# Optimization experiments

Measured on AMD Instinct MI355X. Metric: run time of the kernel, lower is better.

## Reference

```python
import jax, jax.numpy as jnp
import numpy as np
import math

NH, NKV, HD = 8, 1, 128
SOFTCAP = 30.0
ROPE_BASE = 500000.0


def _rope_tables(T, hd, base):
    half = hd // 2
    inv_freq = 1.0 / (base ** (np.arange(half, dtype=np.float32) / half))
    t = np.arange(T, dtype=np.float32)
    ang = np.outer(t, inv_freq)  # [T, half]
    return jnp.asarray(np.cos(ang)), jnp.asarray(np.sin(ang))


def apply_rope(x, cos, sin):
    # x: [B, T, H, hd]; cos/sin: [T, hd//2]
    half = x.shape[-1] // 2
    x1, x2 = x[..., :half], x[..., half:]
    T = x.shape[1]
    c = cos[:T][None, :, None, :]
    s = sin[:T][None, :, None, :]
    return jnp.concatenate([x1 * c - x2 * s, x1 * s + x2 * c], axis=-1)


def setup_inputs() -> dict:
    key = jax.random.key(0)
    ks = jax.random.split(key, 5)
    B, T, D = 4, 2048, 1024
    KD = NKV * HD
    x = jax.random.normal(ks[0], (B, T, D), dtype=jnp.float32)
    Wq = jax.random.normal(ks[1], (D, D), dtype=jnp.float32) * (D ** -0.5)
    Wk = jax.random.normal(ks[2], (KD, D), dtype=jnp.float32) * (D ** -0.5)
    Wv = jax.random.normal(ks[3], (KD, D), dtype=jnp.float32) * (D ** -0.5)
    Wo = jax.random.normal(ks[4], (D, D), dtype=jnp.float32) * (D ** -0.5)
    qk_gain = jnp.full((NH,), 1.5, dtype=jnp.float32)  # qk_gain_init
    cos, sin = _rope_tables(T, HD, ROPE_BASE)
    return {"x": x, "Wq": Wq, "Wk": Wk, "Wv": Wv, "Wo": Wo,
            "qk_gain": qk_gain, "cos": cos, "sin": sin}


def reference(x, Wq, Wk, Wv, Wo, qk_gain, cos, sin):
    B, T, D = x.shape
    # projections (QuantLinear with qat disabled == plain linear, no bias)
    q = (x @ Wq.T).reshape(B, T, NH, HD)
    k = (x @ Wk.T).reshape(B, T, NKV, HD)
    v = (x @ Wv.T).reshape(B, T, NKV, HD)
    q = apply_rope(q, cos, sin)
    k = apply_rope(k, cos, sin)
    # learned per-head QK gain applied to queries
    q = q * qk_gain[None, None, :, 1 - 1][..., None] if False else q * qk_gain[None, None, :, None]
    # GQA: broadcast the single kv head across NH query heads
    scale = 1.0 / math.sqrt(HD)
    scores = jnp.einsum('bqhd,bkgd->bhqk', q, k) * scale  # g==NKV==1 broadcast
    # logit softcap before masking/softmax
    scores = SOFTCAP * jnp.tanh(scores / SOFTCAP)
    causal = jnp.tril(jnp.ones((T, T), dtype=bool))
    scores = jnp.where(causal[None, None], scores, -jnp.inf)
    attn = jax.nn.softmax(scores, axis=-1)  # [B, NH, T, T]
    out = jnp.einsum('bhqk,bkgd->bqhd', attn, v).reshape(B, T, NH * HD)
    return out @ Wo.T
```

## Files before the change

kernel.cpp:

```cpp
#include <hip/hip_runtime.h>
#include <hip/hip_bf16.h>

#define B_ 4
#define T_ 2048
#define D_ 1024
#define NH_ 8
#define HD_ 128

typedef short short8 __attribute__((ext_vector_type(8)));
typedef float floatx4 __attribute__((ext_vector_type(4)));

#if __has_builtin(__builtin_amdgcn_exp2f)
#define EXP2F __builtin_amdgcn_exp2f
#else
#define EXP2F exp2f
#endif
#if __has_builtin(__builtin_amdgcn_rcpf)
#define RCPF __builtin_amdgcn_rcpf
#else
__device__ __forceinline__ float RCPF(float x) { return 1.f / x; }
#endif

#if __has_builtin(__builtin_amdgcn_global_load_lds)
#define G2L(gp, lp)                                                        \
  __builtin_amdgcn_global_load_lds(                                        \
      (const __attribute__((address_space(1))) unsigned int*)(gp),         \
      (__attribute__((address_space(3))) unsigned int*)(lp), 16, 0, 0)
#else
#define G2L(gp, lp) (*(uint4*)(lp) = *(const uint4*)(gp))
#endif

__device__ __forceinline__ unsigned short f2b(float f) {
  union { float fl; unsigned int i; } v; v.fl = f;
  unsigned int r = v.i + 0x7fffu + ((v.i >> 16) & 1u);
  return (unsigned short)(r >> 16);
}
__device__ __forceinline__ unsigned int pack_bf16(float a, float b) {
  unsigned int ua = __float_as_uint(a) + 0x8000u;
  unsigned int ub = __float_as_uint(b) + 0x8000u;
  return (ua >> 16) | (ub & 0xffff0000u);
}
__device__ __forceinline__ float blo(unsigned int u) { return __uint_as_float(u << 16); }
__device__ __forceinline__ float bhi(unsigned int u) { return __uint_as_float(u & 0xffff0000u); }

__global__ __launch_bounds__(256) void cvt_kernel(
    const float* __restrict__ x,  const float* __restrict__ wq,
    const float* __restrict__ wk, const float* __restrict__ wv,
    const float* __restrict__ wo, unsigned short* __restrict__ dst)
{
  size_t i = ((size_t)blockIdx.x * 256 + threadIdx.x) * 8;
  const float* src; size_t off;
  if      (i <  8388608u) { src = x;  off = i; }
  else if (i <  9437184u) { src = wq; off = i - 8388608u; }
  else if (i <  9568256u) { src = wk; off = i - 9437184u; }
  else if (i <  9699328u) { src = wv; off = i - 9568256u; }
  else                    { src = wo; off = i - 9699328u; }
  float4 a = *(const float4*)(src + off);
  float4 b = *(const float4*)(src + off + 4);
  uint4 o;
  o.x = pack_bf16(a.x, a.y); o.y = pack_bf16(a.z, a.w);
  o.z = pack_bf16(b.x, b.y); o.w = pack_bf16(b.z, b.w);
  *(uint4*)(dst + i) = o;
}

template <bool C_F32>
__device__ __forceinline__ void gemm_body_1024(
    const unsigned short* __restrict__ Arow0,
    const unsigned short* __restrict__ Btile,
    void* __restrict__ Cb, int ldC)
{
  __shared__ unsigned short As[128 * 32];
  __shared__ unsigned short Bs[128 * 32];
  const int tid = threadIdx.x;
  const int lane = tid & 63;
  const int w = tid >> 6;
  const int wr = w >> 1, wc = w & 1;
  const int l15 = lane & 15, quad = lane >> 4;

  const unsigned short* a_src = Arow0 + (size_t)(tid >> 2) * 1024 + (tid & 3) * 8;
  const unsigned short* b_src = Btile + (size_t)(tid >> 2) * 1024 + (tid & 3) * 8;
  unsigned short* a_dst = &As[(tid >> 2) * 32 + (tid & 3) * 8];
  unsigned short* b_dst = &Bs[(tid >> 2) * 32 + (tid & 3) * 8];

  floatx4 zero = {0.f, 0.f, 0.f, 0.f};
  floatx4 acc[4][4];
#pragma unroll
  for (int i = 0; i < 4; i++)
#pragma unroll
    for (int j = 0; j < 4; j++) acc[i][j] = zero;

  for (int k0 = 0; k0 < 1024; k0 += 32) {
    __syncthreads();
    G2L(a_src + k0,         a_dst);
    G2L(a_src + 65536 + k0, a_dst + 2048);
    G2L(b_src + k0,         b_dst);
    G2L(b_src + 65536 + k0, b_dst + 2048);
    __syncthreads();
    short8 af[4], bfr[4];
#pragma unroll
    for (int i = 0; i < 4; i++)
      af[i] = *(const short8*)&As[(wr * 64 + i * 16 + l15) * 32 + quad * 8];
#pragma unroll
    for (int j = 0; j < 4; j++)
      bfr[j] = *(const short8*)&Bs[(wc * 64 + j * 16 + l15) * 32 + quad * 8];
#pragma unroll
    for (int i = 0; i < 4; i++)
#pragma unroll
      for (int j = 0; j < 4; j++)
        acc[i][j] = __builtin_amdgcn_mfma_f32_16x16x32_bf16(af[i], bfr[j], acc[i][j], 0, 0, 0);
  }
#pragma unroll
  for (int i = 0; i < 4; i++)
#pragma unroll
    for (int j = 0; j < 4; j++)
#pragma unroll
      for (int r = 0; r < 4; r++) {
        size_t off = (size_t)(wr * 64 + i * 16 + quad * 4 + r) * ldC + wc * 64 + j * 16 + l15;
        if (C_F32) ((float*)Cb)[off] = acc[i][j][r];
        else ((unsigned short*)Cb)[off] = f2b(acc[i][j][r]);
      }
}

__global__ __launch_bounds__(256) void gemm_qkv_kernel(
    const unsigned short* __restrict__ x,
    const unsigned short* __restrict__ Wq,
    const unsigned short* __restrict__ Wk,
    const unsigned short* __restrict__ Wv,
    unsigned short* __restrict__ q,
    unsigned short* __restrict__ k,
    unsigned short* __restrict__ v)
{
  const int bx = blockIdx.x, by = blockIdx.y;
  const unsigned short* Btile;
  unsigned short* C;
  int ldC, col0;
  if (by < 8) { Btile = Wq + (size_t)by * 128 * 1024; C = q; ldC = 1024; col0 = by * 128; }
  else if (by == 8) { Btile = Wk; C = k; ldC = 128; col0 = 0; }
  else { Btile = Wv; C = v; ldC = 128; col0 = 0; }
  gemm_body_1024<false>(x + (size_t)bx * 128 * 1024, Btile,
                        C + (size_t)bx * 128 * ldC + col0, ldC);
}

__global__ __launch_bounds__(256) void gemm_out_kernel(
    const unsigned short* __restrict__ ao,
    const unsigned short* __restrict__ Wo,
    float* __restrict__ out)
{
  const int bx = blockIdx.x, by = blockIdx.y;
  gemm_body_1024<true>(ao + (size_t)bx * 128 * 1024, Wo + (size_t)by * 128 * 1024,
                       out + (size_t)bx * 128 * 1024 + by * 128, 1024);
}

__global__ __launch_bounds__(256) void prep_kernel(
    unsigned short* __restrict__ q,
    unsigned short* __restrict__ k,
    const unsigned short* __restrict__ v,
    unsigned short* __restrict__ vT,
    const float* __restrict__ cosT,
    const float* __restrict__ sinT,
    const float* __restrict__ gain)
{
  __shared__ unsigned short tile[32 * 136];
  const int tid = threadIdx.x;
  if (blockIdx.x < 256) {
    const int b = blockIdx.x >> 6, t0 = (blockIdx.x & 63) * 32;
    for (int u = tid; u < 512; u += 256) {
      int r = u >> 4, c = u & 15;
      *(uint4*)&tile[r * 136 + c * 8] =
          *(const uint4*)(v + ((size_t)(b * T_ + t0 + r)) * 128 + c * 8);
    }
    __syncthreads();
    for (int u = tid; u < 512; u += 256) {
      int d = u >> 2, c = u & 3;
      short8 val;
#pragma unroll
      for (int j = 0; j < 8; j++) val[j] = (short)tile[(c * 8 + j) * 136 + d];
      *(short8*)(vT + ((size_t)(b * 128 + d)) * T_ + t0 + c * 8) = val;
    }
    return;
  }
  int idx = (blockIdx.x - 256) * 256 + tid;
  unsigned short* ptr;
  size_t base;
  int t, j;
  float g;
  if (idx < 524288) {
    j = idx & 7;
    int h = (idx >> 3) & 7;
    int bt = idx >> 6;
    t = bt & (T_ - 1);
    base = (size_t)bt * 1024 + h * 128 + j * 8;
    ptr = q;
    g = gain[h] * 0.0029462782549439484f;
  } else {
    int id = idx - 524288;
    j = id & 7;
    int bt = id >> 3;
    t = bt & (T_ - 1);
    base = (size_t)bt * 128 + j * 8;
    ptr = k;
    g = 1.f;
  }
  float4 ca = *(const float4*)&cosT[t * 64 + j * 8];
  float4 cb = *(const float4*)&cosT[t * 64 + j * 8 + 4];
  float4 sa = *(const float4*)&sinT[t * 64 + j * 8];
  float4 sb = *(const float4*)&sinT[t * 64 + j * 8 + 4];
  uint4 lo = *(const uint4*)(ptr + base);
  uint4 hi = *(const uint4*)(ptr + base + 64);
  uint4 olo, ohi;
  {
    float a0 = blo(lo.x), a1 = bhi(lo.x), b0 = blo(hi.x), b1 = bhi(hi.x);
    olo.x = pack_bf16((a0 * ca.x - b0 * sa.x) * g, (a1 * ca.y - b1 * sa.y) * g);
    ohi.x = pack_bf16((a0 * sa.x + b0 * ca.x) * g, (a1 * sa.y + b1 * ca.y) * g);
  }
  {
    float a0 = blo(lo.y), a1 = bhi(lo.y), b0 = blo(hi.y), b1 = bhi(hi.y);
    olo.y = pack_bf16((a0 * ca.z - b0 * sa.z) * g, (a1 * ca.w - b1 * sa.w) * g);
    ohi.y = pack_bf16((a0 * sa.z + b0 * ca.z) * g, (a1 * sa.w + b1 * ca.w) * g);
  }
  {
    float a0 = blo(lo.z), a1 = bhi(lo.z), b0 = blo(hi.z), b1 = bhi(hi.z);
    olo.z = pack_bf16((a0 * cb.x - b0 * sb.x) * g, (a1 * cb.y - b1 * sb.y) * g);
    ohi.z = pack_bf16((a0 * sb.x + b0 * cb.x) * g, (a1 * sb.y + b1 * cb.y) * g);
  }
  {
    float a0 = blo(lo.w), a1 = bhi(lo.w), b0 = blo(hi.w), b1 = bhi(hi.w);
    olo.w = pack_bf16((a0 * cb.z - b0 * sb.z) * g, (a1 * cb.w - b1 * sb.w) * g);
    ohi.w = pack_bf16((a0 * sb.z + b0 * cb.z) * g, (a1 * sb.w + b1 * cb.w) * g);
  }
  *(uint4*)(ptr + base) = olo;
  *(uint4*)(ptr + base + 64) = ohi;
}

template <int NSPLIT>
__global__ __launch_bounds__(256) void attn_kernel(
    const unsigned short* __restrict__ q,
    const unsigned short* __restrict__ k,
    const unsigned short* __restrict__ vT,
    unsigned short* __restrict__ ao,
    unsigned short* __restrict__ Opart,
    float* __restrict__ lbuf)
{
  __shared__ unsigned short Ks[16 * 264];
  __shared__ unsigned short Vts[128 * 40];
  __shared__ unsigned short Pw[4][32 * 40];

  const int h = blockIdx.y, b = blockIdx.z;
  const int pr   = blockIdx.x / NSPLIT;
  const int part = blockIdx.x % NSPLIT;
  const int tid = threadIdx.x, lane = tid & 63, w = tid >> 6;
  const int l15 = lane & 15, quad = lane >> 4;

  const unsigned short* ksrc =
      k + (size_t)b * T_ * 128 + (size_t)(tid >> 4) * 128 + (tid & 15) * 8;
  unsigned short* kdst0 = &Ks[(tid & 15) * 264 + (tid >> 4) * 8];
  unsigned short* kdst1 = kdst0 + 16 * 8;
  const unsigned short* vsrc =
      vT + (size_t)b * 128 * T_ + (size_t)(tid >> 2) * T_ + (tid & 3) * 8;
  unsigned short* vdst0 = &Vts[(tid >> 2) * 40 + (tid & 3) * 8];
  unsigned short* vdst1 = vdst0 + 64 * 40;

  const floatx4 zero = {0.f, 0.f, 0.f, 0.f};

  for (int pass = 0; pass < 2; pass++) {
    const int qblock = pass ? (15 - pr) : pr;
    const int qbase = qblock * 128;
    const int qw = qbase + w * 32;
    const int seg = (4 * qblock + 4) / NSPLIT;
    const int ktBeg = part * seg, ktEnd = ktBeg + seg;

    short8 qf[2][4];
#pragma unroll
    for (int g = 0; g < 2; g++) {
      const unsigned short* qrow =
          q + ((size_t)(b * T_ + qw + g * 16 + l15) * NH_ + h) * HD_;
#pragma unroll
      for (int c = 0; c < 4; c++) qf[g][c] = *(const short8*)(qrow + c * 32 + quad * 8);
    }

    float l_i[2] = {0.f, 0.f};
    floatx4 acc[8][2];
#pragma unroll
    for (int d = 0; d < 8; d++) { acc[d][0] = zero; acc[d][1] = zero; }

    uint4 kr0 = *(const uint4*)(ksrc + (size_t)ktBeg * 4096);
    uint4 kr1 = *(const uint4*)(ksrc + (size_t)ktBeg * 4096 + 2048);
    uint4 vr0 = *(const uint4*)(vsrc + ktBeg * 32);
    uint4 vr1 = *(const uint4*)(vsrc + (size_t)64 * T_ + ktBeg * 32);

    for (int kt = ktBeg; kt < ktEnd; kt++) {
      __syncthreads();
      *(uint4*)kdst0 = kr0; *(uint4*)kdst1 = kr1;
      *(uint4*)vdst0 = vr0; *(uint4*)vdst1 = vr1;
      int ktn = (kt + 1 < ktEnd) ? kt + 1 : kt;
      kr0 = *(const uint4*)(ksrc + (size_t)ktn * 4096);
      kr1 = *(const uint4*)(ksrc + (size_t)ktn * 4096 + 2048);
      vr0 = *(const uint4*)(vsrc + ktn * 32);
      vr1 = *(const uint4*)(vsrc + (size_t)64 * T_ + ktn * 32);
      __syncthreads();

      if (kt * 32 <= qw + 31) {
        floatx4 st[2][2] = {{zero, zero}, {zero, zero}};
#pragma unroll
        for (int c = 0; c < 4; c++) {
          const int dg = (c * 4 + quad) * 264;
          short8 kf0 = *(const short8*)&Ks[dg + l15 * 8];
          short8 kf1 = *(const short8*)&Ks[dg + (16 + l15) * 8];
          st[0][0] = __builtin_amdgcn_mfma_f32_16x16x32_bf16(kf0, qf[0][c], st[0][0], 0, 0, 0);
          st[0][1] = __builtin_amdgcn_mfma_f32_16x16x32_bf16(kf0, qf[1][c], st[0][1], 0, 0, 0);
          st[1][0] = __builtin_amdgcn_mfma_f32_16x16x32_bf16(kf1, qf[0][c], st[1][0], 0, 0, 0);
          st[1][1] = __builtin_amdgcn_mfma_f32_16x16x32_bf16(kf1, qf[1][c], st[1][1], 0, 0, 0);
        }
        float rs[2] = {0.f, 0.f};
#pragma unroll
        for (int f = 0; f < 2; f++)
#pragma unroll
          for (int g = 0; g < 2; g++) {
            float pv[4];
            const int qrow = qw + g * 16 + l15;
#pragma unroll
            for (int r = 0; r < 4; r++) {
              float s = st[f][g][r];
              float e = EXP2F(2.8853901f * s);
              float u = RCPF(e + 1.f);
              float p = EXP2F(-86.561707f * u);
              int key = kt * 32 + f * 16 + quad * 4 + r;
              p = (key <= qrow) ? p : 0.f;
              pv[r] = p;
              rs[g] += p;
            }
            uint2 pk;
            pk.x = pack_bf16(pv[0], pv[1]);
            pk.y = pack_bf16(pv[2], pv[3]);
            *(uint2*)&Pw[w][(g * 16 + l15) * 40 + f * 16 + quad * 4] = pk;
          }
#pragma unroll
        for (int g = 0; g < 2; g++) {
          float r2 = rs[g] + __shfl_xor(rs[g], 16);
          l_i[g] += r2 + __shfl_xor(r2, 32);
        }
        asm volatile("s_waitcnt lgkmcnt(0)" ::: "memory");
        short8 pf0 = *(const short8*)&Pw[w][l15 * 40 + quad * 8];
        short8 pf1 = *(const short8*)&Pw[w][(16 + l15) * 40 + quad * 8];
#pragma unroll
        for (int d = 0; d < 8; d++) {
          short8 vf = *(const short8*)&Vts[(d * 16 + l15) * 40 + quad * 8];
          acc[d][0] = __builtin_amdgcn_mfma_f32_16x16x32_bf16(vf, pf0, acc[d][0], 0, 0, 0);
          acc[d][1] = __builtin_amdgcn_mfma_f32_16x16x32_bf16(vf, pf1, acc[d][1], 0, 0, 0);
        }
      }
    }

#pragma unroll
    for (int g = 0; g < 2; g++) {
      const size_t rowidx = (size_t)(b * T_ + qw + g * 16 + l15) * NH_ + h;
      if (NSPLIT == 1) {
        float linv = 1.f / l_i[g];
        unsigned short* aop = ao + rowidx * HD_ + quad * 4;
#pragma unroll
        for (int d = 0; d < 8; d++) {
          uint2 o;
          o.x = pack_bf16(acc[d][g][0] * linv, acc[d][g][1] * linv);
          o.y = pack_bf16(acc[d][g][2] * linv, acc[d][g][3] * linv);
          *(uint2*)(aop + d * 16) = o;
        }
      } else {
        unsigned short* dst =
            ((part == NSPLIT - 1) ? ao : Opart + (size_t)part * 8388608u) +
            rowidx * HD_ + quad * 4;
#pragma unroll
        for (int d = 0; d < 8; d++) {
          uint2 o;
          o.x = pack_bf16(acc[d][g][0], acc[d][g][1]);
          o.y = pack_bf16(acc[d][g][2], acc[d][g][3]);
          *(uint2*)(dst + d * 16) = o;
        }
        if (quad == 0) lbuf[(size_t)part * 65536u + rowidx] = l_i[g];
      }
    }
  }
}

template <int NSPLIT>
__global__ __launch_bounds__(256) void combine_kernel(
    const unsigned short* __restrict__ Opart,
    const float* __restrict__ lbuf,
    unsigned short* __restrict__ ao)
{
  size_t i = ((size_t)blockIdx.x * 256 + threadIdx.x) * 8;
  size_t r = i >> 7;
  float ls = 0.f;
#pragma unroll
  for (int p = 0; p < NSPLIT; p++) ls += lbuf[(size_t)p * 65536u + r];
  float linv = RCPF(ls);
  uint4 c = *(const uint4*)(ao + i);
  float v0 = blo(c.x), v1 = bhi(c.x), v2 = blo(c.y), v3 = bhi(c.y);
  float v4 = blo(c.z), v5 = bhi(c.z), v6 = blo(c.w), v7 = bhi(c.w);
#pragma unroll
  for (int p = 0; p < NSPLIT - 1; p++) {
    uint4 a = *(const uint4*)(Opart + (size_t)p * 8388608u + i);
    v0 += blo(a.x); v1 += bhi(a.x); v2 += blo(a.y); v3 += bhi(a.y);
    v4 += blo(a.z); v5 += bhi(a.z); v6 += blo(a.w); v7 += bhi(a.w);
  }
  uint4 o;
  o.x = pack_bf16(v0 * linv, v1 * linv);
  o.y = pack_bf16(v2 * linv, v3 * linv);
  o.z = pack_bf16(v4 * linv, v5 * linv);
  o.w = pack_bf16(v6 * linv, v7 * linv);
  *(uint4*)(ao + i) = o;
}

extern "C" void kernel_launch(void* const* d_in, const int* in_sizes, int n_in,
                              void* d_out, int out_size, void* d_ws, size_t ws_size,
                              hipStream_t stream) {
  const float* x    = (const float*)d_in[0];
  const float* Wq   = (const float*)d_in[1];
  const float* Wk   = (const float*)d_in[2];
  const float* Wv   = (const float*)d_in[3];
  const float* Wo   = (const float*)d_in[4];
  const float* gain = (const float*)d_in[5];
  const float* cosT = (const float*)d_in[6];
  const float* sinT = (const float*)d_in[7];
  float* out = (float*)d_out;

  unsigned short* ws = (unsigned short*)d_ws;
  unsigned short* blob = ws;
  unsigned short* xb  = blob;
  unsigned short* Wqb = blob + 8388608u;
  unsigned short* Wkb = blob + 9437184u;
  unsigned short* Wvb = blob + 9568256u;
  unsigned short* Wob = blob + 9699328u;
  unsigned short* q   = ws + 10747904u;
  unsigned short* kk  = ws + 19136512u;
  unsigned short* v   = ws + 20185088u;
  unsigned short* vT  = ws + 21233664u;
  unsigned short* ao  = xb;
  unsigned short* Opart = ws + 22282240u;
  float* l2 = (float*)((char*)d_ws + 61341696u);
  float* l4 = (float*)((char*)d_ws + 94896128u);
  const size_t need2 = 61865984ull;
  const size_t need4 = 95944704ull;

  cvt_kernel<<<5248, 256, 0, stream>>>(x, Wq, Wk, Wv, Wo, blob);
  gemm_qkv_kernel<<<dim3(64, 10), 256, 0, stream>>>(xb, Wqb, Wkb, Wvb, q, kk, v);
  prep_kernel<<<2560, 256, 0, stream>>>(q, kk, v, vT, cosT, sinT, gain);
  if (ws_size >= need4) {
    attn_kernel<4><<<dim3(32, 8, 4), 256, 0, stream>>>(q, kk, vT, ao, Opart, l4);
    combine_kernel<4><<<4096, 256, 0, stream>>>(Opart, l4, ao);
  } else if (ws_size >= need2) {
    attn_kernel<2><<<dim3(16, 8, 4), 256, 0, stream>>>(q, kk, vT, ao, Opart, l2);
    combine_kernel<2><<<4096, 256, 0, stream>>>(Opart, l2, ao);
  } else {
    attn_kernel<1><<<dim3(8, 8, 4), 256, 0, stream>>>(q, kk, vT, ao, Opart, l2);
  }
  gemm_out_kernel<<<dim3(64, 8), 256, 0, stream>>>(ao, Wob, out);
}
```

Measured before the change: 254.5 us.

## Use 512-thread attention blocks with paired causal query tiles per block

Adds an attention kernel with 512 threads (8 waves) per block. Each block covers 256 query rows and runs two passes over a mirrored pair of query blocks (pr and 7-pr), which balances causal work across blocks. Each K/V tile staged in LDS is shared by twice as many waves, and the grid is halved. The cost is fewer blocks in flight, higher register and LDS use per block, and a serial second pass inside each block.

```diff
diff --git a/kernel.cpp b/kernel.cpp
--- a/kernel.cpp
+++ b/kernel.cpp
@@ -232,6 +232,135 @@
   *(uint4*)(ptr + base + 64) = ohi;
 }
 
+__global__ __launch_bounds__(512) void attn512_kernel(
+    const unsigned short* __restrict__ q,
+    const unsigned short* __restrict__ k,
+    const unsigned short* __restrict__ vT,
+    unsigned short* __restrict__ ao,
+    unsigned short* __restrict__ Opart,
+    float* __restrict__ lbuf)
+{
+  __shared__ unsigned short Ks[16 * 264];
+  __shared__ unsigned short Vts[128 * 40];
+  __shared__ unsigned short Pw[8][32 * 40];
+
+  const int h = blockIdx.y, b = blockIdx.z;
+  const int pr = blockIdx.x >> 2, part = blockIdx.x & 3;
+  const int tid = threadIdx.x, lane = tid & 63, w = tid >> 6;
+  const int l15 = lane & 15, quad = lane >> 4;
+
+  const unsigned short* ksrc =
+      k + (size_t)b * T_ * 128 + (size_t)(tid >> 4) * 128 + (tid & 15) * 8;
+  unsigned short* kdst = &Ks[(tid & 15) * 264 + (tid >> 4) * 8];
+  const unsigned short* vsrc =
+      vT + (size_t)b * 128 * T_ + (size_t)(tid >> 2) * T_ + (tid & 3) * 8;
+  unsigned short* vdst = &Vts[(tid >> 2) * 40 + (tid & 3) * 8];
+
+  const floatx4 zero = {0.f, 0.f, 0.f, 0.f};
+
+  for (int pass = 0; pass < 2; pass++) {
+    const int qblock = pass ? (7 - pr) : pr;
+    const int qbase = qblock * 256;
+    const int qw = qbase + w * 32;
+    const int seg = 2 * qblock + 2;
+    const int ktBeg = part * seg, ktEnd = ktBeg + seg;
+
+    short8 qf[2][4];
+#pragma unroll
+    for (int g = 0; g < 2; g++) {
+      const unsigned short* qrow =
+          q + ((size_t)(b * T_ + qw + g * 16 + l15) * NH_ + h) * HD_;
+#pragma unroll
+      for (int c = 0; c < 4; c++) qf[g][c] = *(const short8*)(qrow + c * 32 + quad * 8);
+    }
+
+    float l_i[2] = {0.f, 0.f};
+    floatx4 acc[8][2];
+#pragma unroll
+    for (int d = 0; d < 8; d++) { acc[d][0] = zero; acc[d][1] = zero; }
+
+    uint4 kr = *(const uint4*)(ksrc + (size_t)ktBeg * 4096);
+    uint4 vr = *(const uint4*)(vsrc + ktBeg * 32);
+
+    for (int kt = ktBeg; kt < ktEnd; kt++) {
+      __syncthreads();
+      *(uint4*)kdst = kr;
+      *(uint4*)vdst = vr;
+      int ktn = (kt + 1 < ktEnd) ? kt + 1 : kt;
+      kr = *(const uint4*)(ksrc + (size_t)ktn * 4096);
+      vr = *(const uint4*)(vsrc + ktn * 32);
+      __syncthreads();
+
+      if (kt * 32 <= qw + 31) {
+        floatx4 st[2][2] = {{zero, zero}, {zero, zero}};
+#pragma unroll
+        for (int c = 0; c < 4; c++) {
+          const int dg = (c * 4 + quad) * 264;
+          short8 kf0 = *(const short8*)&Ks[dg + l15 * 8];
+          short8 kf1 = *(const short8*)&Ks[dg + (16 + l15) * 8];
+          st[0][0] = __builtin_amdgcn_mfma_f32_16x16x32_bf16(kf0, qf[0][c], st[0][0], 0, 0, 0);
+          st[0][1] = __builtin_amdgcn_mfma_f32_16x16x32_bf16(kf0, qf[1][c], st[0][1], 0, 0, 0);
+          st[1][0] = __builtin_amdgcn_mfma_f32_16x16x32_bf16(kf1, qf[0][c], st[1][0], 0, 0, 0);
+          st[1][1] = __builtin_amdgcn_mfma_f32_16x16x32_bf16(kf1, qf[1][c], st[1][1], 0, 0, 0);
+        }
+        float rs[2] = {0.f, 0.f};
+#pragma unroll
+        for (int f = 0; f < 2; f++)
+#pragma unroll
+          for (int g = 0; g < 2; g++) {
+            float pv[4];
+            const int qrow = qw + g * 16 + l15;
+#pragma unroll
+            for (int r = 0; r < 4; r++) {
+              float s = st[f][g][r];
+              float e = EXP2F(2.8853901f * s);
+              float u = RCPF(e + 1.f);
+              float p = EXP2F(-86.561707f * u);
+              int key = kt * 32 + f * 16 + quad * 4 + r;
+              p = (key <= qrow) ? p : 0.f;
+              pv[r] = p;
+              rs[g] += p;
+            }
+            uint2 pk;
+            pk.x = pack_bf16(pv[0], pv[1]);
+            pk.y = pack_bf16(pv[2], pv[3]);
+            *(uint2*)&Pw[w][(g * 16 + l15) * 40 + f * 16 + quad * 4] = pk;
+          }
+#pragma unroll
+        for (int g = 0; g < 2; g++) {
+          float r2 = rs[g] + __shfl_xor(rs[g], 16);
+          l_i[g] += r2 + __shfl_xor(r2, 32);
+        }
+        asm volatile("s_waitcnt lgkmcnt(0)" ::: "memory");
+        short8 pf0 = *(const short8*)&Pw[w][l15 * 40 + quad * 8];
+        short8 pf1 = *(const short8*)&Pw[w][(16 + l15) * 40 + quad * 8];
+#pragma unroll
+        for (int d = 0; d < 8; d++) {
+          short8 vf = *(const short8*)&Vts[(d * 16 + l15) * 40 + quad * 8];
+          acc[d][0] = __builtin_amdgcn_mfma_f32_16x16x32_bf16(vf, pf0, acc[d][0], 0, 0, 0);
+          acc[d][1] = __builtin_amdgcn_mfma_f32_16x16x32_bf16(vf, pf1, acc[d][1], 0, 0, 0);
+        }
+      }
+    }
+
+#pragma unroll
+    for (int g = 0; g < 2; g++) {
+      const size_t rowidx = (size_t)(b * T_ + qw + g * 16 + l15) * NH_ + h;
+      unsigned short* dst =
+          ((part == 3) ? ao : Opart + (size_t)part * 8388608u) +
+          rowidx * HD_ + quad * 4;
+#pragma unroll
+      for (int d = 0; d < 8; d++) {
+        uint2 o;
+        o.x = pack_bf16(acc[d][g][0], acc[d][g][1]);
+        o.y = pack_bf16(acc[d][g][2], acc[d][g][3]);
+        *(uint2*)(dst + d * 16) = o;
+      }
+      if (quad == 0) lbuf[(size_t)part * 65536u + rowidx] = l_i[g];
+    }
+  }
+}
+
 template <int NSPLIT>
 __global__ __launch_bounds__(256) void attn_kernel(
     const unsigned short* __restrict__ q,
@@ -445,7 +574,7 @@
   gemm_qkv_kernel<<<dim3(64, 10), 256, 0, stream>>>(xb, Wqb, Wkb, Wvb, q, kk, v);
   prep_kernel<<<2560, 256, 0, stream>>>(q, kk, v, vT, cosT, sinT, gain);
   if (ws_size >= need4) {
-    attn_kernel<4><<<dim3(32, 8, 4), 256, 0, stream>>>(q, kk, vT, ao, Opart, l4);
+    attn512_kernel<<<dim3(16, 8, 4), 512, 0, stream>>>(q, kk, vT, ao, Opart, l4);
     combine_kernel<4><<<4096, 256, 0, stream>>>(Opart, l4, ao);
   } else if (ws_size >= need2) {
     attn_kernel<2><<<dim3(16, 8, 4), 256, 0, stream>>>(q, kk, vT, ao, Opart, l2);
```

New measurement: 261.4 us. 2.7% more time.

## Double-buffer K/V tiles in LDS, skip masking on full tiles, drop 4-way split

Applied to the files above, without the earlier changes.

Keeps two LDS buffers for the K and V^T tiles so the next tile can be written while the current one is consumed, which removes one of the two barriers per key tile. Adds a fast path that skips the causal mask compare on tiles lying fully below the diagonal. Removes the 4-way key-split attention path, so the 2-way split (or no split) is now used. This lowers the number of blocks and the combine traffic, but may reduce parallelism, and the larger LDS footprint may reduce occupancy.

```diff
diff --git a/kernel.cpp b/kernel.cpp
--- a/kernel.cpp
+++ b/kernel.cpp
@@ -241,8 +241,8 @@
     unsigned short* __restrict__ Opart,
     float* __restrict__ lbuf)
 {
-  __shared__ unsigned short Ks[16 * 264];
-  __shared__ unsigned short Vts[128 * 40];
+  __shared__ unsigned short Ks[2][16 * 264];
+  __shared__ unsigned short Vts[2][128 * 40];
   __shared__ unsigned short Pw[4][32 * 40];
 
   const int h = blockIdx.y, b = blockIdx.z;
@@ -253,12 +253,12 @@
 
   const unsigned short* ksrc =
       k + (size_t)b * T_ * 128 + (size_t)(tid >> 4) * 128 + (tid & 15) * 8;
-  unsigned short* kdst0 = &Ks[(tid & 15) * 264 + (tid >> 4) * 8];
-  unsigned short* kdst1 = kdst0 + 16 * 8;
+  const int koff0 = (tid & 15) * 264 + (tid >> 4) * 8;
+  const int koff1 = koff0 + 16 * 8;
   const unsigned short* vsrc =
       vT + (size_t)b * 128 * T_ + (size_t)(tid >> 2) * T_ + (tid & 3) * 8;
-  unsigned short* vdst0 = &Vts[(tid >> 2) * 40 + (tid & 3) * 8];
-  unsigned short* vdst1 = vdst0 + 64 * 40;
+  const int voff0 = (tid >> 2) * 40 + (tid & 3) * 8;
+  const int voff1 = voff0 + 64 * 40;
 
   const floatx4 zero = {0.f, 0.f, 0.f, 0.f};
 
@@ -283,57 +283,94 @@
 #pragma unroll
     for (int d = 0; d < 8; d++) { acc[d][0] = zero; acc[d][1] = zero; }
 
-    uint4 kr0 = *(const uint4*)(ksrc + (size_t)ktBeg * 4096);
-    uint4 kr1 = *(const uint4*)(ksrc + (size_t)ktBeg * 4096 + 2048);
-    uint4 vr0 = *(const uint4*)(vsrc + ktBeg * 32);
-    uint4 vr1 = *(const uint4*)(vsrc + (size_t)64 * T_ + ktBeg * 32);
+    __syncthreads();
+    {
+      uint4 kr0 = *(const uint4*)(ksrc + (size_t)ktBeg * 4096);
+      uint4 kr1 = *(const uint4*)(ksrc + (size_t)ktBeg * 4096 + 2048);
+      uint4 vr0 = *(const uint4*)(vsrc + ktBeg * 32);
+      uint4 vr1 = *(const uint4*)(vsrc + (size_t)64 * T_ + ktBeg * 32);
+      unsigned short* kb = Ks[ktBeg & 1];
+      unsigned short* vb = Vts[ktBeg & 1];
+      *(uint4*)(kb + koff0) = kr0; *(uint4*)(kb + koff1) = kr1;
+      *(uint4*)(vb + voff0) = vr0; *(uint4*)(vb + voff1) = vr1;
+    }
 
     for (int kt = ktBeg; kt < ktEnd; kt++) {
+      uint4 kr0, kr1, vr0, vr1;
+      const bool more = (kt + 1 < ktEnd);
+      if (more) {
+        kr0 = *(const uint4*)(ksrc + (size_t)(kt + 1) * 4096);
+        kr1 = *(const uint4*)(ksrc + (size_t)(kt + 1) * 4096 + 2048);
+        vr0 = *(const uint4*)(vsrc + (kt + 1) * 32);
+        vr1 = *(const uint4*)(vsrc + (size_t)64 * T_ + (kt + 1) * 32);
+      }
       __syncthreads();
-      *(uint4*)kdst0 = kr0; *(uint4*)kdst1 = kr1;
-      *(uint4*)vdst0 = vr0; *(uint4*)vdst1 = vr1;
-      int ktn = (kt + 1 < ktEnd) ? kt + 1 : kt;
-      kr0 = *(const uint4*)(ksrc + (size_t)ktn * 4096);
-      kr1 = *(const uint4*)(ksrc + (size_t)ktn * 4096 + 2048);
-      vr0 = *(const uint4*)(vsrc + ktn * 32);
-      vr1 = *(const uint4*)(vsrc + (size_t)64 * T_ + ktn * 32);
-      __syncthreads();
+      if (more) {
+        unsigned short* kb = Ks[(kt + 1) & 1];
+        unsigned short* vb = Vts[(kt + 1) & 1];
+        *(uint4*)(kb + koff0) = kr0; *(uint4*)(kb + koff1) = kr1;
+        *(uint4*)(vb + voff0) = vr0; *(uint4*)(vb + voff1) = vr1;
+      }
 
       if (kt * 32 <= qw + 31) {
+        const unsigned short* KsC = Ks[kt & 1];
+        const unsigned short* VtC = Vts[kt & 1];
         floatx4 st[2][2] = {{zero, zero}, {zero, zero}};
 #pragma unroll
         for (int c = 0; c < 4; c++) {
           const int dg = (c * 4 + quad) * 264;
-          short8 kf0 = *(const short8*)&Ks[dg + l15 * 8];
-          short8 kf1 = *(const short8*)&Ks[dg + (16 + l15) * 8];
+          short8 kf0 = *(const short8*)&KsC[dg + l15 * 8];
+          short8 kf1 = *(const short8*)&KsC[dg + (16 + l15) * 8];
           st[0][0] = __builtin_amdgcn_mfma_f32_16x16x32_bf16(kf0, qf[0][c], st[0][0], 0, 0, 0);
           st[0][1] = __builtin_amdgcn_mfma_f32_16x16x32_bf16(kf0, qf[1][c], st[0][1], 0, 0, 0);
           st[1][0] = __builtin_amdgcn_mfma_f32_16x16x32_bf16(kf1, qf[0][c], st[1][0], 0, 0, 0);
           st[1][1] = __builtin_amdgcn_mfma_f32_16x16x32_bf16(kf1, qf[1][c], st[1][1], 0, 0, 0);
         }
         float rs[2] = {0.f, 0.f};
-#pragma unroll
-        for (int f = 0; f < 2; f++)
-#pragma unroll
-          for (int g = 0; g < 2; g++) {
-            float pv[4];
-            const int qrow = qw + g * 16 + l15;
-#pragma unroll
-            for (int r = 0; r < 4; r++) {
-              float s = st[f][g][r];
-              float e = EXP2F(2.8853901f * s);
-              float u = RCPF(e + 1.f);
-              float p = EXP2F(-86.561707f * u);
-              int key = kt * 32 + f * 16 + quad * 4 + r;
-              p = (key <= qrow) ? p : 0.f;
-              pv[r] = p;
-              rs[g] += p;
+        if (kt * 32 + 31 <= qw) {
+#pragma unroll
+          for (int f = 0; f < 2; f++)
+#pragma unroll
+            for (int g = 0; g < 2; g++) {
+              float pv[4];
+#pragma unroll
+              for (int r = 0; r < 4; r++) {
+                float s = st[f][g][r];
+                float e = EXP2F(2.8853901f * s);
+                float u = RCPF(e + 1.f);
+                float p = EXP2F(-86.561707f * u);
+                pv[r] = p;
+                rs[g] += p;
+              }
+              uint2 pk;
+              pk.x = pack_bf16(pv[0], pv[1]);
+              pk.y = pack_bf16(pv[2], pv[3]);
+              *(uint2*)&Pw[w][(g * 16 + l15) * 40 + f * 16 + quad * 4] = pk;
             }
-            uint2 pk;
-            pk.x = pack_bf16(pv[0], pv[1]);
-            pk.y = pack_bf16(pv[2], pv[3]);
-            *(uint2*)&Pw[w][(g * 16 + l15) * 40 + f * 16 + quad * 4] = pk;
-          }
+        } else {
+#pragma unroll
+          for (int f = 0; f < 2; f++)
+#pragma unroll
+            for (int g = 0; g < 2; g++) {
+              float pv[4];
+              const int qrow = qw + g * 16 + l15;
+#pragma unroll
+              for (int r = 0; r < 4; r++) {
+                float s = st[f][g][r];
+                float e = EXP2F(2.8853901f * s);
+                float u = RCPF(e + 1.f);
+                float p = EXP2F(-86.561707f * u);
+                int key = kt * 32 + f * 16 + quad * 4 + r;
+                p = (key <= qrow) ? p : 0.f;
+                pv[r] = p;
+                rs[g] += p;
+              }
+              uint2 pk;
+              pk.x = pack_bf16(pv[0], pv[1]);
+              pk.y = pack_bf16(pv[2], pv[3]);
+              *(uint2*)&Pw[w][(g * 16 + l15) * 40 + f * 16 + quad * 4] = pk;
+            }
+        }
 #pragma unroll
         for (int g = 0; g < 2; g++) {
           float r2 = rs[g] + __shfl_xor(rs[g], 16);
@@ -344,7 +381,7 @@
         short8 pf1 = *(const short8*)&Pw[w][(16 + l15) * 40 + quad * 8];
 #pragma unroll
         for (int d = 0; d < 8; d++) {
-          short8 vf = *(const short8*)&Vts[(d * 16 + l15) * 40 + quad * 8];
+          short8 vf = *(const short8*)&VtC[(d * 16 + l15) * 40 + quad * 8];
           acc[d][0] = __builtin_amdgcn_mfma_f32_16x16x32_bf16(vf, pf0, acc[d][0], 0, 0, 0);
           acc[d][1] = __builtin_amdgcn_mfma_f32_16x16x32_bf16(vf, pf1, acc[d][1], 0, 0, 0);
         }
@@ -437,17 +474,12 @@
   unsigned short* ao  = xb;
   unsigned short* Opart = ws + 22282240u;
   float* l2 = (float*)((char*)d_ws + 61341696u);
-  float* l4 = (float*)((char*)d_ws + 94896128u);
   const size_t need2 = 61865984ull;
-  const size_t need4 = 95944704ull;
 
   cvt_kernel<<<5248, 256, 0, stream>>>(x, Wq, Wk, Wv, Wo, blob);
   gemm_qkv_kernel<<<dim3(64, 10), 256, 0, stream>>>(xb, Wqb, Wkb, Wvb, q, kk, v);
   prep_kernel<<<2560, 256, 0, stream>>>(q, kk, v, vT, cosT, sinT, gain);
-  if (ws_size >= need4) {
-    attn_kernel<4><<<dim3(32, 8, 4), 256, 0, stream>>>(q, kk, vT, ao, Opart, l4);
-    combine_kernel<4><<<4096, 256, 0, stream>>>(Opart, l4, ao);
-  } else if (ws_size >= need2) {
+  if (ws_size >= need2) {
     attn_kernel<2><<<dim3(16, 8, 4), 256, 0, stream>>>(q, kk, vT, ao, Opart, l2);
     combine_kernel<2><<<4096, 256, 0, stream>>>(Opart, l2, ao);
   } else {
```

New measurement: 233.4 us. 8.3% less time.
